# Kernel optimization log

Measured on AMD Instinct MI355X. Metric: run time of the kernel, lower is better.

## Reference

```python
import jax, jax.numpy as jnp
import numpy as np

CONF_THRES = 0.25
IOU_THRES = 0.45
MAX_DET = 300      # max detections returned (padded/masked to static shape)
K = 8192           # top-K score candidates entering NMS (static bound)
N_ANCHORS = 102000 # YOLOv5 @ 1280px
NC = 80            # COCO classes


def setup_inputs() -> dict:
    key = jax.random.key(0)
    # [B=1, N, 4 (xywh) + 1 (obj) + 80 (cls)] raw head predictions in [0,1)
    preds = jax.random.uniform(key, (1, N_ANCHORS, 4 + 1 + NC), dtype=jnp.float32)
    return {"preds": preds}


def _xywh2yxyx(b):
    # (xc, yc, w, h) -> (y1, x1, y2, x2), matching pt_xywh2yxyx_yolo
    x, y, w, h = b[..., 0], b[..., 1], b[..., 2], b[..., 3]
    return jnp.stack([y - h * 0.5, x - w * 0.5, y + h * 0.5, x + w * 0.5], axis=-1)


def _iou_matrix(boxes):
    # boxes: [K, 4] in yxyx; returns pairwise IoU [K, K]
    area = (boxes[:, 2] - boxes[:, 0]) * (boxes[:, 3] - boxes[:, 1])
    ty = jnp.maximum(boxes[:, None, 0], boxes[None, :, 0])
    tx = jnp.maximum(boxes[:, None, 1], boxes[None, :, 1])
    by = jnp.minimum(boxes[:, None, 2], boxes[None, :, 2])
    bx = jnp.minimum(boxes[:, None, 3], boxes[None, :, 3])
    inter = jnp.clip(by - ty, 0.0) * jnp.clip(bx - tx, 0.0)
    union = area[:, None] + area[None, :] - inter
    return inter / (union + 1e-9)


def _yolo_nms(preds):
    p = preds[0]                       # [N, 85] (loop returns on first image)
    obj = p[:, 4]                      # objectness
    cand = obj > CONF_THRES            # confidence filter
    cls_scores = p[:, 5:] * obj[:, None]
    scores = jnp.max(cls_scores, axis=1)
    classes = jnp.argmax(cls_scores, axis=1).astype(jnp.float32)
    scores = jnp.where(cand, scores, 0.0)  # mask instead of dynamic filter
    boxes = _xywh2yxyx(p[:, :4])       # [N, 4] yxyx

    # top-K candidates by score (static replacement for boolean filtering)
    top_scores, idx = jax.lax.top_k(scores, K)
    top_boxes = boxes[idx]
    top_classes = classes[idx]
    valid = top_scores > 0.0

    iou = _iou_matrix(top_boxes)       # [K, K], 256 MB fp32

    # greedy NMS: boxes already sorted by descending score
    ar = jnp.arange(K)

    def body(i, suppressed):
        keep_i = jnp.logical_and(jnp.logical_not(suppressed[i]), valid[i])
        return suppressed | (keep_i & (iou[i] > IOU_THRES) & (ar > i))

    suppressed = jax.lax.fori_loop(0, K, body, jnp.zeros((K,), jnp.bool_))
    keep = valid & jnp.logical_not(suppressed)

    # gather top MAX_DET kept detections (sorted), zero-pad the rest
    keep_scores = jnp.where(keep, top_scores, -1.0)
    _, sel = jax.lax.top_k(keep_scores, MAX_DET)
    mask = keep[sel]
    out_boxes = jnp.where(mask[:, None], top_boxes[sel], 0.0)[None]    # [1, MAX_DET, 4]
    out_classes = jnp.where(mask, top_classes[sel], 0.0)[None]         # [1, MAX_DET]
    out_scores = jnp.where(mask, top_scores[sel], 0.0)[None]           # [1, MAX_DET]
    return out_boxes, out_classes, out_scores


def reference(preds):
    return _yolo_nms(preds)
```

## Files before the change

kernel.cpp:

```cpp
#include <hip/hip_runtime.h>
#include <cstdint>

#define CONF_THRES 0.25f
#define IOU_THRES  0.45f
#define MAX_DET    300
#define K_TOP      8192
#define NA         102000
#define NCLS       80
#define ROWLEN     85
#define CAP        32640
#define NPLANE     32
#define WIN        512
#define NWIN       (K_TOP / WIN)
#define SSTR       9

typedef unsigned long long u64;
typedef unsigned int u32;

__global__ __launch_bounds__(256) void score_key_kernel(const float* __restrict__ preds,
        u64* __restrict__ keys, u32* __restrict__ histP) {
#pragma clang fp contract(off)
    int lane = threadIdx.x & 63;
    int i = blockIdx.x * 4 + (threadIdx.x >> 6);
    if (i >= NA) return;
    const float* p = preds + (size_t)i * ROWLEN;
    float v0 = p[lane];
    float v1 = (lane < ROWLEN - 64) ? p[64 + lane] : 0.0f;
    float obj = __shfl(v0, 4);
    float m = (lane >= 5) ? v0 : 0.0f;
    m = fmaxf(m, (lane < 21) ? v1 : 0.0f);
    for (int off = 32; off; off >>= 1) m = fmaxf(m, __shfl_xor(m, off));
    if (lane == 0) {
        float score = (obj > CONF_THRES) ? m * obj : 0.0f;
        u32 sb = __float_as_uint(score);
        keys[i] = ((u64)sb << 32) | (u32)(~(u32)i);
        if (sb != 0u)
            atomicAdd(&histP[((u32)blockIdx.x & (NPLANE - 1u)) * 65536u + (sb >> 16)], 1u);
    }
}

__global__ __launch_bounds__(256) void reduce_hist_kernel(const u32* __restrict__ histP,
        u32* __restrict__ sumhist) {
    int bin = blockIdx.x * 256 + threadIdx.x;
    u32 s = 0;
#pragma unroll
    for (int r = 0; r < NPLANE; ++r) s += histP[r * 65536 + bin];
    sumhist[bin] = s;
}

__global__ __launch_bounds__(1024) void cutoff_kernel(const u32* __restrict__ hist,
        u32* __restrict__ meta) {
    __shared__ u32 suf[1024];
    __shared__ int cbs;
    __shared__ u32 above_s;
    int t = threadIdx.x;
    u32 s = 0;
    const u32* hb = hist + t * 64;
    for (int b = 0; b < 64; ++b) s += hb[b];
    suf[t] = s;
    if (t == 0) { cbs = -1; above_s = 0; }
    __syncthreads();
    for (int off = 1; off < 1024; off <<= 1) {
        u32 add = (t + off < 1024) ? suf[t + off] : 0u;
        __syncthreads();
        suf[t] += add;
        __syncthreads();
    }
    u32 st = suf[t];
    u32 stn = (t < 1023) ? suf[t + 1] : 0u;
    if (st >= (u32)K_TOP && stn < (u32)K_TOP) {
        cbs = t;
        above_s = stn;
    }
    __syncthreads();
    int cb = cbs;
    if (t < 64) {
        u32 thresh = 0;
        if (cb >= 0) {
            u32 above = above_s;
            u32 v = hist[cb * 64 + t];
            for (int off = 1; off < 64; off <<= 1) {
                u32 o = __shfl_down(v, off);
                if (t + off < 64) v += o;
            }
            u64 bal = __ballot(v + above >= (u32)K_TOP);
            int bstar = 63 - __builtin_clzll((unsigned long long)bal);
            thresh = ((u32)(cb * 64 + bstar)) << 16;
        }
        if (t == 0) meta[1] = thresh;
    }
}

__global__ __launch_bounds__(256) void compact_kernel(const u64* __restrict__ keys,
        u32* __restrict__ meta, u64* __restrict__ comp) {
    __shared__ u32 woff[4];
    __shared__ u32 bbase;
    int i = blockIdx.x * 256 + threadIdx.x;
    int wid = threadIdx.x >> 6, lane = threadIdx.x & 63;
    u64 key = (i < NA) ? keys[i] : 0ull;
    u32 sb = (u32)(key >> 32);
    u32 th = meta[1];
    bool take = (i < NA) && (sb != 0u) && (sb >= th);
    u64 bal = __ballot(take);
    if (lane == 0) woff[wid] = (u32)__popcll(bal);
    __syncthreads();
    if (threadIdx.x == 0) {
        u32 t0 = woff[0], t1 = woff[1], t2 = woff[2], t3 = woff[3];
        bbase = atomicAdd(&meta[0], t0 + t1 + t2 + t3);
        woff[0] = 0; woff[1] = t0; woff[2] = t0 + t1; woff[3] = t0 + t1 + t2;
    }
    __syncthreads();
    if (take) {
        u32 pos = bbase + woff[wid] + (u32)__popcll(bal & ((1ull << lane) - 1ull));
        if (pos < CAP) comp[pos] = key;
    }
}

__global__ __launch_bounds__(256) void rank_partial_kernel(const u64* __restrict__ comp,
        const u32* __restrict__ meta, u32* __restrict__ rankArr) {
    __shared__ u64 tile[1024];
    u32 cnt = meta[0];
    int n = (int)(cnt < (u32)CAP ? cnt : (u32)CAP);
    int i0 = blockIdx.x * 256;
    int j0 = blockIdx.y * 1024;
    if (i0 >= n || j0 >= n) return;
    int lim = n - j0; if (lim > 1024) lim = 1024;
    for (int k = threadIdx.x; k < 1024; k += 256)
        tile[k] = (k < lim) ? comp[j0 + k] : 0ull;
    __syncthreads();
    int i = i0 + threadIdx.x;
    if (i < n) {
        u64 key = comp[i];
        u32 r = 0;
#pragma unroll 8
        for (int j = 0; j < 1024; ++j) r += (tile[j] > key) ? 1u : 0u;
        atomicAdd(&rankArr[i], r);
    }
}

__global__ __launch_bounds__(256) void scatter_kernel(const u64* __restrict__ comp,
        const u32* __restrict__ meta, const u32* __restrict__ rankArr,
        u64* __restrict__ sorted) {
    u32 cnt = meta[0];
    int n = (int)(cnt < (u32)CAP ? cnt : (u32)CAP);
    int i = blockIdx.x * 256 + threadIdx.x;
    if (i < n) {
        u32 r = rankArr[i];
        if (r < (u32)K_TOP) sorted[r] = comp[i];
    }
}

__global__ __launch_bounds__(256) void gather_kernel(const u64* __restrict__ sorted,
        const float* __restrict__ preds, float* __restrict__ boxes,
        float* __restrict__ scores, float* __restrict__ classes) {
#pragma clang fp contract(off)
    int lane = threadIdx.x & 63;
    int i = blockIdx.x * 4 + (threadIdx.x >> 6);
    u64 key = sorted[i];
    u32 sb = (u32)(key >> 32);
    float score = __uint_as_float(sb);
    if (score > 0.0f) {
        u32 idx = ~(u32)(key & 0xffffffffull);
        const float* p = preds + (size_t)idx * ROWLEN;
        float v0 = p[lane];
        float v1 = (lane < ROWLEN - 64) ? p[64 + lane] : 0.0f;
        float obj = __shfl(v0, 4);
        u64 kb = 0;
        if (lane >= 5) {
            float q = v0 * obj;
            kb = ((u64)__float_as_uint(q) << 8) | (u32)(255 - (lane - 5));
        }
        if (lane < 21) {
            float q = v1 * obj;
            u64 kb2 = ((u64)__float_as_uint(q) << 8) | (u32)(255 - (59 + lane));
            if (kb2 > kb) kb = kb2;
        }
        for (int off = 32; off; off >>= 1) {
            u64 o = __shfl_xor(kb, off);
            if (o > kb) kb = o;
        }
        u32 cls = 255u - (u32)(kb & 0xffull);
        float x = __shfl(v0, 0), y = __shfl(v0, 1);
        float w = __shfl(v0, 2), h = __shfl(v0, 3);
        if (lane == 0) {
            boxes[i * 4 + 0] = y - h * 0.5f;
            boxes[i * 4 + 1] = x - w * 0.5f;
            boxes[i * 4 + 2] = y + h * 0.5f;
            boxes[i * 4 + 3] = x + w * 0.5f;
            scores[i] = score;
            classes[i] = (float)cls;
        }
    } else if (lane == 0) {
        boxes[i * 4 + 0] = 0.0f; boxes[i * 4 + 1] = 0.0f;
        boxes[i * 4 + 2] = 0.0f; boxes[i * 4 + 3] = 0.0f;
        scores[i] = 0.0f;
        classes[i] = 0.0f;
    }
}

__global__ __launch_bounds__(256) void mask_kernel(const float* __restrict__ boxes,
        u64* __restrict__ mask) {
#pragma clang fp contract(off)
    __shared__ float4 sbox[1024 + 16];
    int ct = blockIdx.x;
    int rb = blockIdx.y;
    int t = threadIdx.x;
    for (int jj = t; jj < 1024; jj += 256)
        sbox[jj + (jj >> 6)] = ((const float4*)boxes)[ct * 1024 + jj];
    __syncthreads();
    int r = rb * 16 + (t >> 4);
    int wq = t & 15;
    int j0g = ct * 1024 + wq * 64;
    float4 bi = ((const float4*)boxes)[r];
    float area_i = (bi.z - bi.x) * (bi.w - bi.y);
    u64 bits = 0;
    if (j0g + 63 > r) {
        for (int k = 0; k < 64; ++k) {
            int j = j0g + k;
            if (j <= r) continue;
            float4 bj = sbox[wq * 65 + k];
            float area_j = (bj.z - bj.x) * (bj.w - bj.y);
            float ty = fmaxf(bi.x, bj.x);
            float tx = fmaxf(bi.y, bj.y);
            float by = fminf(bi.z, bj.z);
            float bx = fminf(bi.w, bj.w);
            float inter = fmaxf(by - ty, 0.0f) * fmaxf(bx - tx, 0.0f);
            float uni = (area_i + area_j) - inter;
            float iou = inter / (uni + 1e-9f);
            if (iou > IOU_THRES) bits |= (1ull << k);
        }
    }
    mask[(size_t)r * 128 + ct * 16 + wq] = bits;
}

__global__ __launch_bounds__(256) void valid_kernel(const float* __restrict__ scores,
        u64* __restrict__ remw) {
    int w = blockIdx.x * 4 + (threadIdx.x >> 6);
    int lane = threadIdx.x & 63;
    u64 b = __ballot(scores[w * 64 + lane] > 0.0f);
    if (lane == 0) remw[w] = b;
}

__device__ __forceinline__ u64 rfl64(u64 v) {
    u32 lo = (u32)__builtin_amdgcn_readfirstlane((int)(u32)v);
    u32 hi = (u32)__builtin_amdgcn_readfirstlane((int)(u32)(v >> 32));
    return ((u64)hi << 32) | lo;
}

__device__ __forceinline__ u64 bcast64(u64 v, int srclane) {
    u32 lo = (u32)__builtin_amdgcn_readlane((int)(u32)v, srclane);
    u32 hi = (u32)__builtin_amdgcn_readlane((int)(u32)(v >> 32), srclane);
    return ((u64)hi << 32) | lo;
}

__device__ __forceinline__ u64 shfl_xor64(u64 v, int m) {
    u32 lo = __shfl_xor((u32)v, m, 64);
    u32 hi = __shfl_xor((u32)(v >> 32), m, 64);
    return ((u64)hi << 32) | lo;
}

__global__ __launch_bounds__(64) void nms_scan_kernel(const u64* __restrict__ mask,
        const u64* __restrict__ remw, const float* __restrict__ boxes,
        const float* __restrict__ scores, const float* __restrict__ classes,
        float* __restrict__ out) {
    __shared__ u64 sub[WIN * SSTR];
    __shared__ u32 ki[MAX_DET + 8];
    int lane = threadIdx.x;
    int n = 0;
    for (int win = 0; win < NWIN && n < MAX_DET; ++win) {
        int rbase = win * WIN;
        __syncthreads();
#pragma unroll 8
        for (int it = 0; it < 32; ++it) {
            int idx = it * 64 + lane;
            int r = idx >> 2, j = (idx & 3) * 2;
            uint4 v = *(const uint4*)&mask[(size_t)(rbase + r) * 128 + win * 8 + j];
            sub[r * SSTR + j]     = ((u64)v.y << 32) | v.x;
            sub[r * SSTR + j + 1] = ((u64)v.w << 32) | v.z;
        }
        u64 acc[8] = {0, 0, 0, 0, 0, 0, 0, 0};
        for (int m = lane; m < n; m += 64) {
            int k = (int)ki[m];
            const u64* rp = &mask[(size_t)k * 128 + win * 8];
#pragma unroll
            for (int j = 0; j < 8; ++j) acc[j] |= rp[j];
        }
#pragma unroll
        for (int j = 0; j < 8; ++j)
            for (int off = 32; off; off >>= 1) acc[j] |= shfl_xor64(acc[j], off);
        __syncthreads();
        u64 diag[8];
#pragma unroll
        for (int sw = 0; sw < 8; ++sw) diag[sw] = sub[(sw * 64 + lane) * SSTR + sw];
        int n0 = n;
        u64 keptW[8] = {0, 0, 0, 0, 0, 0, 0, 0};
#pragma unroll
        for (int sw = 0; sw < 8; ++sw) {
            if (n < MAX_DET) {
                u64 acc2 = 0;
#pragma unroll
                for (int wp = 0; wp < 8; ++wp) {
                    if (wp < sw) {
                        if ((keptW[wp] >> lane) & 1ull)
                            acc2 |= sub[(wp * 64 + lane) * SSTR + sw];
                    }
                }
                for (int off = 32; off; off >>= 1) acc2 |= shfl_xor64(acc2, off);
                u64 cur = rfl64(remw[win * 8 + sw]) & ~rfl64(acc[sw]) & ~rfl64(acc2);
                u64 kw = 0;
                while (cur != 0ull && n < MAX_DET) {
                    int b = __ffsll((unsigned long long)cur) - 1;
                    u64 slice = bcast64(diag[sw], b);
                    kw |= (1ull << b);
                    cur &= ~(slice | (1ull << b));
                    ++n;
                }
                keptW[sw] = kw;
            }
        }
        int base = n0;
#pragma unroll
        for (int sw = 0; sw < 8; ++sw) {
            u64 kw = keptW[sw];
            if ((kw >> lane) & 1ull) {
                int rr = (int)__popcll(kw & ((1ull << lane) - 1ull));
                ki[base + rr] = (u32)(rbase + sw * 64 + lane);
            }
            base += (int)__popcll(kw);
        }
        __syncthreads();
    }
    __syncthreads();
    for (int m = lane; m < MAX_DET; m += 64) {
        float4 b = make_float4(0.0f, 0.0f, 0.0f, 0.0f);
        float c = 0.0f, s = 0.0f;
        if (m < n) {
            int k = (int)ki[m];
            b = ((const float4*)boxes)[k];
            c = classes[k];
            s = scores[k];
        }
        ((float4*)out)[m] = b;
        out[1200 + m] = c;
        out[1500 + m] = s;
    }
}

extern "C" void kernel_launch(void* const* d_in, const int* in_sizes, int n_in,
                              void* d_out, int out_size, void* d_ws, size_t ws_size,
                              hipStream_t stream) {
    const float* preds = (const float*)d_in[0];
    char* ws = (char*)d_ws;

    u32*   sumhist = (u32*)(ws + 0);
    u32*   meta    = (u32*)(ws + 262144);
    u64*   remw    = (u64*)(ws + 262208);
    u64*   sorted  = (u64*)(ws + 263232);
    u64*   keys    = (u64*)(ws + 328768);
    u32*   rankArr = (u32*)(ws + 328768);
    u64*   comp    = (u64*)(ws + 1144768);
    float* tboxes  = (float*)(ws + 1405888);
    float* tscores = (float*)(ws + 1536960);
    float* tclass  = (float*)(ws + 1569728);
    u64*   mask    = (u64*)(ws + 1602496);
    u32*   histP   = (u32*)(ws + 1602496);
    float* out     = (float*)d_out;

    hipMemsetAsync(ws, 0, 328768, stream);
    hipMemsetAsync(histP, 0, (size_t)NPLANE * 65536 * 4, stream);

    score_key_kernel<<<(NA + 3) / 4, 256, 0, stream>>>(preds, keys, histP);
    reduce_hist_kernel<<<256, 256, 0, stream>>>(histP, sumhist);
    cutoff_kernel<<<1, 1024, 0, stream>>>(sumhist, meta);
    compact_kernel<<<(NA + 255) / 256, 256, 0, stream>>>(keys, meta, comp);
    hipMemsetAsync(rankArr, 0, (size_t)CAP * 4, stream);
    rank_partial_kernel<<<dim3((CAP + 255) / 256, (CAP + 1023) / 1024), 256, 0, stream>>>(
            comp, meta, rankArr);
    scatter_kernel<<<(CAP + 255) / 256, 256, 0, stream>>>(comp, meta, rankArr, sorted);
    gather_kernel<<<K_TOP / 4, 256, 0, stream>>>(sorted, preds, tboxes, tscores, tclass);
    mask_kernel<<<dim3(8, 512), 256, 0, stream>>>(tboxes, mask);
    valid_kernel<<<32, 256, 0, stream>>>(tscores, remw);
    nms_scan_kernel<<<1, 64, 0, stream>>>(mask, remw, tboxes, tscores, tclass, out);
}
```

Before: 228.9 us.

## Restructure IoU mask kernel: 64-row lane mapping, precomputed areas, division-free threshold

The IoU mask kernel now gives each lane one row, so a wavefront reads the same column box from shared memory as a broadcast. Each thread covers four 64-column words, and the grid shrinks from 512 to 128 row blocks. Column areas are precomputed once into shared memory. The IoU comparison skips the divide when the value is clearly above or below the threshold, falling back to the exact division only in a narrow band. Results are staged in a padded shared tile and written out with 128-bit coalesced stores, at the cost of a second barrier and more shared memory per block.

```diff
diff --git a/kernel.cpp b/kernel.cpp
--- a/kernel.cpp
+++ b/kernel.cpp
@@ -201,36 +201,60 @@
 __global__ __launch_bounds__(256) void mask_kernel(const float* __restrict__ boxes,
         u64* __restrict__ mask) {
 #pragma clang fp contract(off)
-    __shared__ float4 sbox[1024 + 16];
+    __shared__ float4 sbox[1024];
+    __shared__ float sarea[1024];
+    __shared__ u64 wtile[64 * 17];
     int ct = blockIdx.x;
     int rb = blockIdx.y;
     int t = threadIdx.x;
-    for (int jj = t; jj < 1024; jj += 256)
-        sbox[jj + (jj >> 6)] = ((const float4*)boxes)[ct * 1024 + jj];
-    __syncthreads();
-    int r = rb * 16 + (t >> 4);
-    int wq = t & 15;
-    int j0g = ct * 1024 + wq * 64;
+    for (int jj = t; jj < 1024; jj += 256) {
+        float4 b = ((const float4*)boxes)[ct * 1024 + jj];
+        sbox[jj] = b;
+        sarea[jj] = (b.z - b.x) * (b.w - b.y);
+    }
+    __syncthreads();
+    int lane = t & 63, w = t >> 6;
+    int r = rb * 64 + lane;
     float4 bi = ((const float4*)boxes)[r];
-    float area_i = (bi.z - bi.x) * (bi.w - bi.y);
-    u64 bits = 0;
-    if (j0g + 63 > r) {
-        for (int k = 0; k < 64; ++k) {
-            int j = j0g + k;
-            if (j <= r) continue;
-            float4 bj = sbox[wq * 65 + k];
-            float area_j = (bj.z - bj.x) * (bj.w - bj.y);
-            float ty = fmaxf(bi.x, bj.x);
-            float tx = fmaxf(bi.y, bj.y);
-            float by = fminf(bi.z, bj.z);
-            float bx = fminf(bi.w, bj.w);
-            float inter = fmaxf(by - ty, 0.0f) * fmaxf(bx - tx, 0.0f);
-            float uni = (area_i + area_j) - inter;
-            float iou = inter / (uni + 1e-9f);
-            if (iou > IOU_THRES) bits |= (1ull << k);
-        }
-    }
-    mask[(size_t)r * 128 + ct * 16 + wq] = bits;
+    float ai = (bi.z - bi.x) * (bi.w - bi.y);
+    int rbb = rb * 64;
+#pragma unroll
+    for (int q = 0; q < 4; ++q) {
+        int wq = w + q * 4;
+        int j0g = ct * 1024 + wq * 64;
+        u64 bits = 0;
+        if (j0g + 63 > rbb) {
+            for (int k = 0; k < 64; ++k) {
+                int j = j0g + k;
+                float4 bj = sbox[wq * 64 + k];
+                float aj = sarea[wq * 64 + k];
+                float ty = fmaxf(bi.x, bj.x);
+                float tx = fmaxf(bi.y, bj.y);
+                float by = fminf(bi.z, bj.z);
+                float bx = fminf(bi.w, bj.w);
+                float ih = fmaxf(by - ty, 0.0f);
+                float iw = fmaxf(bx - tx, 0.0f);
+                float inter = ih * iw;
+                float uni = (ai + aj) - inter;
+                float d = uni + 1e-9f;
+                bool kp;
+                if (inter > 0.451f * d) kp = true;
+                else if (inter <= 0.449f * d) kp = false;
+                else kp = (inter / d > IOU_THRES);
+                if (kp && j > r) bits |= (1ull << k);
+            }
+        }
+        wtile[lane * 17 + wq] = bits;
+    }
+    __syncthreads();
+    int rr = t >> 2, wbase = (t & 3) * 4;
+    u64 b0 = wtile[rr * 17 + wbase + 0];
+    u64 b1 = wtile[rr * 17 + wbase + 1];
+    u64 b2 = wtile[rr * 17 + wbase + 2];
+    u64 b3 = wtile[rr * 17 + wbase + 3];
+    u64* dst = &mask[(size_t)(rb * 64 + rr) * 128 + ct * 16 + wbase];
+    *(uint4*)dst = make_uint4((u32)b0, (u32)(b0 >> 32), (u32)b1, (u32)(b1 >> 32));
+    *(uint4*)(dst + 2) = make_uint4((u32)b2, (u32)(b2 >> 32), (u32)b3, (u32)(b3 >> 32));
 }
 
 __global__ __launch_bounds__(256) void valid_kernel(const float* __restrict__ scores,
@@ -378,7 +402,7 @@
             comp, meta, rankArr);
     scatter_kernel<<<(CAP + 255) / 256, 256, 0, stream>>>(comp, meta, rankArr, sorted);
     gather_kernel<<<K_TOP / 4, 256, 0, stream>>>(sorted, preds, tboxes, tscores, tclass);
-    mask_kernel<<<dim3(8, 512), 256, 0, stream>>>(tboxes, mask);
+    mask_kernel<<<dim3(8, 128), 256, 0, stream>>>(tboxes, mask);
     valid_kernel<<<32, 256, 0, stream>>>(tscores, remw);
     nms_scan_kernel<<<1, 64, 0, stream>>>(mask, remw, tboxes, tscores, tclass, out);
 }
```

New measurement: 230.4 us. About the same (+0.6%).
